# Kernel tuning notes

Measured on AMD Instinct MI355X. Metric: run time of the kernel, lower is better.

## Reference

```python
import jax, jax.numpy as jnp
import numpy as np

C, G, S, L, B = 16, 8192, 8, 3, 32


def setup_inputs() -> dict:
    key = jax.random.key(0)
    kx, kI = jax.random.split(key)
    # x: valuation vector over G ground atoms per batch element, in [0,1)
    x = jax.random.uniform(kx, (B, G), dtype=jnp.float32)
    # I: precomputed index tensor [C, G, S, L], indices into the G axis of x
    I = jax.random.randint(kI, (C, G, S, L), 0, G, dtype=jnp.int64)
    return {"x": x, "I": I}


def reference(x, I):
    # Equivalent of: for each clause i, gather(V_tild, 1, I_i) -> prod over L -> sum over S
    # torch gather semantics: out[b, g, s, l] = x[b, I[i, g, s, l]]
    # Vectorized over all clauses at once; no repeat/broadcast materialization beyond the gather.
    gathered = x[:, I]                        # [B, C, G, S, L]
    body = jnp.prod(gathered, axis=-1)        # conjunction over L body literals -> [B, C, G, S]
    clause_val = jnp.sum(body, axis=-1)       # sum over S substitutions -> [B, C, G]
    # torch.stack over clauses puts C first: [C, B, G]
    return jnp.transpose(clause_val, (1, 0, 2))
```

## Files before the change

### kernel.cpp

```cpp
#include <hip/hip_runtime.h>
#include <hip/hip_fp16.h>
#include <stdint.h>

#define Cc 16
#define Gg 8192
#define Ss 8
#define Ll 3
#define Bb 32

#define BH 4
#define NZ (Bb / BH)
#define THREADS 512

__device__ __forceinline__ void clause_eval(const uint2* __restrict__ xl2,
                                            const int4 q[6], float acc[4]) {
    #pragma unroll
    for (int h = 0; h < 2; ++h) {
        const int4 qa = q[3 * h + 0];
        const int4 qb = q[3 * h + 1];
        const int4 qc = q[3 * h + 2];
        int idx[12] = {qa.x, qa.y, qa.z, qa.w,
                       qb.x, qb.y, qb.z, qb.w,
                       qc.x, qc.y, qc.z, qc.w};
        uint2 r[12];
        #pragma unroll
        for (int k = 0; k < 12; ++k)
            r[k] = xl2[(uint32_t)idx[k]];
        #pragma unroll
        for (int s = 0; s < 4; ++s) {
            const uint2 ra = r[3 * s + 0];
            const uint2 rb = r[3 * s + 1];
            const uint2 rd = r[3 * s + 2];
            __half2 p0 = __hmul2(__hmul2(*(const __half2*)&ra.x,
                                         *(const __half2*)&rb.x),
                                 *(const __half2*)&rd.x);
            __half2 p1 = __hmul2(__hmul2(*(const __half2*)&ra.y,
                                         *(const __half2*)&rb.y),
                                 *(const __half2*)&rd.y);
            float2 f0 = __half22float2(p0);
            float2 f1 = __half22float2(p1);
            acc[0] += f0.x;
            acc[1] += f0.y;
            acc[2] += f1.x;
            acc[3] += f1.y;
        }
    }
}

#define EVAL_STORE(QBUF, CVAL, GVAL)                                          \
    {                                                                         \
        float acc[4] = {0.f, 0.f, 0.f, 0.f};                                  \
        clause_eval(xl, QBUF, acc);                                           \
        float* op = out + ((size_t)((CVAL) * Bb + BH * zh)) * Gg + (GVAL);    \
        __builtin_nontemporal_store(acc[0], &op[0]);                          \
        __builtin_nontemporal_store(acc[1], &op[(size_t)Gg]);                 \
        __builtin_nontemporal_store(acc[2], &op[2 * (size_t)Gg]);             \
        __builtin_nontemporal_store(acc[3], &op[3 * (size_t)Gg]);             \
    }

__global__ __launch_bounds__(THREADS, 4) void clause_f16_1r(
        const float* __restrict__ x, const int* __restrict__ I,
        float* __restrict__ out) {
    __shared__ uint2 xl[Gg];
    const int tid = threadIdx.x;

    const int lb = (blockIdx.x & 7) * 64 + (blockIdx.x >> 3);
    const int zh = lb & (NZ - 1);
    const int combo = lb >> 3;
    const int gc = combo & 7;
    const int cp = combo >> 3;
    const int gbase = gc * 1024;
    const int c0 = 2 * cp, c1 = 2 * cp + 1;
    const int g0 = gbase + tid;
    const int g1 = gbase + THREADS + tid;

    const float* xs = x + (size_t)(BH * zh) * Gg;
    float4 v[4][4];
    #pragma unroll
    for (int k = 0; k < 4; ++k) {
        const int g = 4 * tid + k * (4 * THREADS);
        #pragma unroll
        for (int r = 0; r < 4; ++r)
            v[k][r] = *(const float4*)&xs[(size_t)r * Gg + g];
    }

    int4 qA[6], qB[6];
    {
        const int4* ip = (const int4*)(I + ((size_t)c0 * Gg + g0) * (Ss * Ll));
        #pragma unroll
        for (int k = 0; k < 6; ++k) qA[k] = ip[k];
    }

    #pragma unroll
    for (int k = 0; k < 4; ++k) {
        const int g = 4 * tid + k * (4 * THREADS);
        const float4 r0 = v[k][0], r1 = v[k][1], r2 = v[k][2], r3 = v[k][3];
        __half2 l0 = __floats2half2_rn(r0.x, r1.x);
        __half2 h0 = __floats2half2_rn(r2.x, r3.x);
        __half2 l1 = __floats2half2_rn(r0.y, r1.y);
        __half2 h1 = __floats2half2_rn(r2.y, r3.y);
        __half2 l2 = __floats2half2_rn(r0.z, r1.z);
        __half2 h2v = __floats2half2_rn(r2.z, r3.z);
        __half2 l3 = __floats2half2_rn(r0.w, r1.w);
        __half2 h3 = __floats2half2_rn(r2.w, r3.w);
        uint4 w0 = make_uint4(*(const uint32_t*)&l0, *(const uint32_t*)&h0,
                              *(const uint32_t*)&l1, *(const uint32_t*)&h1);
        uint4 w1 = make_uint4(*(const uint32_t*)&l2, *(const uint32_t*)&h2v,
                              *(const uint32_t*)&l3, *(const uint32_t*)&h3);
        *(uint4*)&xl[g] = w0;
        *(uint4*)&xl[g + 2] = w1;
    }

    __syncthreads();

    {
        const int4* ip = (const int4*)(I + ((size_t)c0 * Gg + g1) * (Ss * Ll));
        #pragma unroll
        for (int k = 0; k < 6; ++k) qB[k] = ip[k];
        EVAL_STORE(qA, c0, g0)
    }
    {
        const int4* ip = (const int4*)(I + ((size_t)c1 * Gg + g0) * (Ss * Ll));
        #pragma unroll
        for (int k = 0; k < 6; ++k) qA[k] = ip[k];
        EVAL_STORE(qB, c0, g1)
    }
    {
        const int4* ip = (const int4*)(I + ((size_t)c1 * Gg + g1) * (Ss * Ll));
        #pragma unroll
        for (int k = 0; k < 6; ++k) qB[k] = ip[k];
        EVAL_STORE(qA, c1, g0)
    }
    {
        EVAL_STORE(qB, c1, g1)
    }
}

extern "C" void kernel_launch(void* const* d_in, const int* in_sizes, int n_in,
                              void* d_out, int out_size, void* d_ws, size_t ws_size,
                              hipStream_t stream) {
    const float* x = (const float*)d_in[0];
    const int* I = (const int*)d_in[1];
    float* out = (float*)d_out;
    (void)d_ws; (void)ws_size;

    const int grid = 512;
    clause_f16_1r<<<grid, THREADS, 0, stream>>>(x, I, out);
}
```

Measured before the change: 80.55 us.

## Add prepass compressing indices to 16-bit and pre-packing x as fp16

Adds a prepass kernel that converts the int32 index tensor to packed 16-bit indices and the x rows to interleaved fp16 in workspace. The main kernel then loads pre-packed x straight into LDS and issues all four index loads up front, so the eight batch-group blocks re-read half as many index bytes. This adds a second launch and a full read/write pass over I on every call. A plain direct kernel is used as a fallback when the workspace is too small.

After: 78.91 us. 2.0% less time.

```diff
diff --git a/kernel.cpp b/kernel.cpp
--- a/kernel.cpp
+++ b/kernel.cpp
@@ -10,22 +10,67 @@
 
 #define BH 4
 #define NZ (Bb / BH)
-#define THREADS 512
+#define MTHREADS 512
 
-__device__ __forceinline__ void clause_eval(const uint2* __restrict__ xl2,
-                                            const int4 q[6], float acc[4]) {
+#define XH_BYTES  ((size_t)NZ * Gg * BH * 2)
+#define I16_OFF   XH_BYTES
+#define I16_BYTES ((size_t)Cc * Gg * Ss * Ll * 2)
+
+#define PB_X 64
+#define PB_I 384
+__global__ __launch_bounds__(256) void prepass(const float* __restrict__ x,
+                                               const uint4* __restrict__ I4,
+                                               uint4* __restrict__ ws4) {
+    const int bid = blockIdx.x;
+    if (bid < PB_X) {
+        const int tt = bid * 256 + threadIdx.x;
+        const int zh = tt >> 11;
+        const int gg = (tt & 2047) << 2;
+        const float* xr = x + (size_t)(4 * zh) * Gg + gg;
+        float4 f0 = *(const float4*)&xr[0];
+        float4 f1 = *(const float4*)&xr[Gg];
+        float4 f2 = *(const float4*)&xr[2 * (size_t)Gg];
+        float4 f3 = *(const float4*)&xr[3 * (size_t)Gg];
+        __half2 lo0 = __floats2half2_rn(f0.x, f1.x), hi0 = __floats2half2_rn(f2.x, f3.x);
+        __half2 lo1 = __floats2half2_rn(f0.y, f1.y), hi1 = __floats2half2_rn(f2.y, f3.y);
+        __half2 lo2 = __floats2half2_rn(f0.z, f1.z), hi2 = __floats2half2_rn(f2.z, f3.z);
+        __half2 lo3 = __floats2half2_rn(f0.w, f1.w), hi3 = __floats2half2_rn(f2.w, f3.w);
+        uint4 w0 = make_uint4(*(uint32_t*)&lo0, *(uint32_t*)&hi0,
+                              *(uint32_t*)&lo1, *(uint32_t*)&hi1);
+        uint4 w1 = make_uint4(*(uint32_t*)&lo2, *(uint32_t*)&hi2,
+                              *(uint32_t*)&lo3, *(uint32_t*)&hi3);
+        uint4* dst = ws4 + ((size_t)zh << 12) + ((size_t)(tt & 2047) << 1);
+        dst[0] = w0;
+        dst[1] = w1;
+    } else {
+        const int t = (bid - PB_X) * 256 + threadIdx.x;
+        uint2* ow = (uint2*)((char*)ws4 + I16_OFF);
+        #pragma unroll
+        for (int i = 0; i < 8; ++i) {
+            const int e = t + i * (PB_I * 256);
+            uint4 v = I4[e];
+            uint2 o;
+            o.x = (v.x & 0xffffu) | (v.y << 16);
+            o.y = (v.z & 0xffffu) | (v.w << 16);
+            ow[e] = o;
+        }
+    }
+}
+
+__device__ __forceinline__ void clause_eval16(const uint2* __restrict__ xl2,
+                                              const uint4 q[3], float acc[4]) {
+    const uint32_t u[12] = {q[0].x, q[0].y, q[0].z, q[0].w,
+                            q[1].x, q[1].y, q[1].z, q[1].w,
+                            q[2].x, q[2].y, q[2].z, q[2].w};
     #pragma unroll
     for (int h = 0; h < 2; ++h) {
-        const int4 qa = q[3 * h + 0];
-        const int4 qb = q[3 * h + 1];
-        const int4 qc = q[3 * h + 2];
-        int idx[12] = {qa.x, qa.y, qa.z, qa.w,
-                       qb.x, qb.y, qb.z, qb.w,
-                       qc.x, qc.y, qc.z, qc.w};
         uint2 r[12];
         #pragma unroll
-        for (int k = 0; k < 12; ++k)
-            r[k] = xl2[(uint32_t)idx[k]];
+        for (int m = 0; m < 6; ++m) {
+            const uint32_t w = u[6 * h + m];
+            r[2 * m]     = xl2[w & 0xffffu];
+            r[2 * m + 1] = xl2[w >> 16];
+        }
         #pragma unroll
         for (int s = 0; s < 4; ++s) {
             const uint2 ra = r[3 * s + 0];
@@ -47,21 +92,28 @@
     }
 }
 
-#define EVAL_STORE(QBUF, CVAL, GVAL)                                          \
+#define QLOAD(QB, CV, GV)                                                     \
+    {                                                                         \
+        const uint4* p =                                                      \
+            (const uint4*)(i16 + ((size_t)(CV) * Gg + (GV)) * (Ss * Ll));     \
+        QB[0] = p[0]; QB[1] = p[1]; QB[2] = p[2];                             \
+    }
+
+#define EVAL_STORE(QB, CV, GV)                                                \
     {                                                                         \
         float acc[4] = {0.f, 0.f, 0.f, 0.f};                                  \
-        clause_eval(xl, QBUF, acc);                                           \
-        float* op = out + ((size_t)((CVAL) * Bb + BH * zh)) * Gg + (GVAL);    \
+        clause_eval16(xl2, QB, acc);                                          \
+        float* op = out + ((size_t)((CV) * Bb + BH * zh)) * Gg + (GV);        \
         __builtin_nontemporal_store(acc[0], &op[0]);                          \
         __builtin_nontemporal_store(acc[1], &op[(size_t)Gg]);                 \
         __builtin_nontemporal_store(acc[2], &op[2 * (size_t)Gg]);             \
         __builtin_nontemporal_store(acc[3], &op[3 * (size_t)Gg]);             \
     }
 
-__global__ __launch_bounds__(THREADS, 4) void clause_f16_1r(
-        const float* __restrict__ x, const int* __restrict__ I,
+__global__ __launch_bounds__(MTHREADS, 4) void clause_m(
+        const uint4* __restrict__ xh4, const ushort* __restrict__ i16,
         float* __restrict__ out) {
-    __shared__ uint2 xl[Gg];
+    __shared__ uint4 xl4[Gg / 2];
     const int tid = threadIdx.x;
 
     const int lb = (blockIdx.x & 7) * 64 + (blockIdx.x >> 3);
@@ -72,68 +124,50 @@
     const int gbase = gc * 1024;
     const int c0 = 2 * cp, c1 = 2 * cp + 1;
     const int g0 = gbase + tid;
-    const int g1 = gbase + THREADS + tid;
+    const int g1 = gbase + MTHREADS + tid;
 
-    const float* xs = x + (size_t)(BH * zh) * Gg;
-    float4 v[4][4];
+    const uint4* src = xh4 + ((size_t)zh << 12);
+    uint4 st[8];
     #pragma unroll
-    for (int k = 0; k < 4; ++k) {
-        const int g = 4 * tid + k * (4 * THREADS);
-        #pragma unroll
-        for (int r = 0; r < 4; ++r)
-            v[k][r] = *(const float4*)&xs[(size_t)r * Gg + g];
-    }
+    for (int i = 0; i < 8; ++i) st[i] = src[tid + i * MTHREADS];
 
-    int4 qA[6], qB[6];
-    {
-        const int4* ip = (const int4*)(I + ((size_t)c0 * Gg + g0) * (Ss * Ll));
-        #pragma unroll
-        for (int k = 0; k < 6; ++k) qA[k] = ip[k];
-    }
+    uint4 qA[3], qB[3], qC[3], qD[3];
+    QLOAD(qA, c0, g0)
+    QLOAD(qB, c0, g1)
+    QLOAD(qC, c1, g0)
+    QLOAD(qD, c1, g1)
 
     #pragma unroll
-    for (int k = 0; k < 4; ++k) {
-        const int g = 4 * tid + k * (4 * THREADS);
-        const float4 r0 = v[k][0], r1 = v[k][1], r2 = v[k][2], r3 = v[k][3];
-        __half2 l0 = __floats2half2_rn(r0.x, r1.x);
-        __half2 h0 = __floats2half2_rn(r2.x, r3.x);
-        __half2 l1 = __floats2half2_rn(r0.y, r1.y);
-        __half2 h1 = __floats2half2_rn(r2.y, r3.y);
-        __half2 l2 = __floats2half2_rn(r0.z, r1.z);
-        __half2 h2v = __floats2half2_rn(r2.z, r3.z);
-        __half2 l3 = __floats2half2_rn(r0.w, r1.w);
-        __half2 h3 = __floats2half2_rn(r2.w, r3.w);
-        uint4 w0 = make_uint4(*(const uint32_t*)&l0, *(const uint32_t*)&h0,
-                              *(const uint32_t*)&l1, *(const uint32_t*)&h1);
-        uint4 w1 = make_uint4(*(const uint32_t*)&l2, *(const uint32_t*)&h2v,
-                              *(const uint32_t*)&l3, *(const uint32_t*)&h3);
-        *(uint4*)&xl[g] = w0;
-        *(uint4*)&xl[g + 2] = w1;
-    }
+    for (int i = 0; i < 8; ++i) xl4[tid + i * MTHREADS] = st[i];
 
     __syncthreads();
 
-    {
-        const int4* ip = (const int4*)(I + ((size_t)c0 * Gg + g1) * (Ss * Ll));
-        #pragma unroll
-        for (int k = 0; k < 6; ++k) qB[k] = ip[k];
-        EVAL_STORE(qA, c0, g0)
+    const uint2* xl2 = (const uint2*)xl4;
+    EVAL_STORE(qA, c0, g0)
+    EVAL_STORE(qB, c0, g1)
+    EVAL_STORE(qC, c1, g0)
+    EVAL_STORE(qD, c1, g1)
+}
+
+__global__ __launch_bounds__(256) void clause_kernel_direct(const float* __restrict__ x,
+                                                            const int* __restrict__ I,
+                                                            float* __restrict__ out) {
+    const int tid = threadIdx.x;
+    const int b = tid & 31;
+    const int j = tid >> 5;
+    const int g = blockIdx.x * 8 + j;
+    const int c = blockIdx.y;
+
+    const int* Icg = I + (size_t)(c * Gg + g) * (Ss * Ll);
+    float sum = 0.f;
+    #pragma unroll
+    for (int s = 0; s < Ss; ++s) {
+        float p0 = x[(size_t)b * Gg + Icg[3 * s + 0]];
+        float p1 = x[(size_t)b * Gg + Icg[3 * s + 1]];
+        float p2 = x[(size_t)b * Gg + Icg[3 * s + 2]];
+        sum += p0 * p1 * p2;
     }
-    {
-        const int4* ip = (const int4*)(I + ((size_t)c1 * Gg + g0) * (Ss * Ll));
-        #pragma unroll
-        for (int k = 0; k < 6; ++k) qA[k] = ip[k];
-        EVAL_STORE(qB, c0, g1)
-    }
-    {
-        const int4* ip = (const int4*)(I + ((size_t)c1 * Gg + g1) * (Ss * Ll));
-        #pragma unroll
-        for (int k = 0; k < 6; ++k) qB[k] = ip[k];
-        EVAL_STORE(qA, c1, g0)
-    }
-    {
-        EVAL_STORE(qB, c1, g1)
-    }
+    out[(size_t)(c * Bb + b) * Gg + g] = sum;
 }
 
 extern "C" void kernel_launch(void* const* d_in, const int* in_sizes, int n_in,
@@ -142,8 +176,14 @@
     const float* x = (const float*)d_in[0];
     const int* I = (const int*)d_in[1];
     float* out = (float*)d_out;
-    (void)d_ws; (void)ws_size;
 
-    const int grid = 512;
-    clause_f16_1r<<<grid, THREADS, 0, stream>>>(x, I, out);
+    const size_t need = I16_OFF + I16_BYTES;
+    if (ws_size >= need) {
+        prepass<<<PB_X + PB_I, 256, 0, stream>>>(x, (const uint4*)I,
+                                                 (uint4*)d_ws);
+        clause_m<<<512, MTHREADS, 0, stream>>>(
+            (const uint4*)d_ws, (const ushort*)((char*)d_ws + I16_OFF), out);
+    } else {
+        clause_kernel_direct<<<dim3(Gg / 8, Cc), 256, 0, stream>>>(x, I, out);
+    }
 }
```
